# Kernel tuning notes

Measured on AMD Instinct MI355X. Metric: run time of the kernel, lower is better.

Reference implementation:

```python
import jax, jax.numpy as jnp
import numpy as np


def setup_inputs() -> dict:
    key = jax.random.key(0)
    kq, kk, kv = jax.random.split(key, 3)
    B, S, D = 8, 2048, 128
    Q = jax.random.normal(kq, (B, S, D), dtype=jnp.float32)
    K = jax.random.normal(kk, (B, S, D), dtype=jnp.float32)
    V = jax.random.normal(kv, (B, S, D), dtype=jnp.float32)
    return {"Q": Q, "K": K, "V": V}


def reference(Q, K, V):
    # scores: [B, S, S]
    d = Q.shape[-1]
    scores = jnp.einsum('bqd,bkd->bqk', Q, K) / jnp.sqrt(jnp.float32(d))
    # causal mask: position i attends to keys <= i (original sets upper triangle to -inf)
    S = scores.shape[-1]
    causal = jnp.tril(jnp.ones((S, S), dtype=bool))  # [S, S]
    scores = jnp.where(causal[None, :, :], scores, -jnp.inf)
    probs = jax.nn.softmax(scores, axis=-1)
    return jnp.einsum('bqk,bkd->bqd', probs, V)
```

## Files before the change

kernel.cpp:

```cpp
#include <hip/hip_runtime.h>

#define BB 8
#define SS 2048
#define DD 128
#define SEG ((size_t)BB * SS * DD)

typedef _Float16 f16;
typedef _Float16 f16x2 __attribute__((ext_vector_type(2)));
typedef __fp16 h16x2 __attribute__((ext_vector_type(2)));
typedef _Float16 f16x8 __attribute__((ext_vector_type(8)));
typedef float f32x4 __attribute__((ext_vector_type(4)));

#define SWV(d) ((((d) & 7) ^ (((d) >> 3) & 7)) << 3)

#define DEFER_THR 4.0f

static __device__ __forceinline__ float fast_exp2(float x) {
#if __has_builtin(__builtin_amdgcn_exp2f)
    return __builtin_amdgcn_exp2f(x);
#else
    return exp2f(x);
#endif
}

static __device__ __forceinline__ f16x2 cvt_pk(float a, float b) {
    h16x2 r = __builtin_amdgcn_cvt_pkrtz(a, b);
    return __builtin_bit_cast(f16x2, r);
}

static __device__ __forceinline__ uint2 pack4(f32x4 v) {
    f16x2 lo = cvt_pk(v[0], v[1]);
    f16x2 hi = cvt_pk(v[2], v[3]);
    uint2 u;
    u.x = __builtin_bit_cast(unsigned int, lo);
    u.y = __builtin_bit_cast(unsigned int, hi);
    return u;
}

template <int NS>
__global__ __launch_bounds__(256, 2)
void attn_fwd(const float* __restrict__ Qg, const float* __restrict__ Kg,
              const float* __restrict__ Vg, float* __restrict__ Og,
              f16* __restrict__ Opf, float2* __restrict__ mlb)
{
    __shared__ __align__(16) f16 Kl[2][64 * 128];
    __shared__ __align__(16) f16 Vt[2][128 * 64];
    __shared__ __align__(16) f16 Pl[4][16 * 64];

    const int tid  = threadIdx.x;
    const int lane = tid & 63;
    const int w    = tid >> 6;
    const int c_   = lane & 15;
    const int g    = lane >> 4;

    const int L   = blockIdx.x;
    const int bb  = L & 7;
    const int rem = L >> 3;
    const int qb  = 31 - (rem / NS);
    const int sg  = rem % NS;
    const int T   = qb + 1;
    const int t0  = (T * sg) / NS;
    const int t1  = (T * (sg + 1)) / NS;

    const int qrow0 = qb * 64 + w * 16;

    const float qs = 0.08838834764831845f * 1.4426950408889634f;
    f16x8 qf[4];
    {
        const float* qp = Qg + (size_t)(bb * SS + qrow0 + c_) * DD;
#pragma unroll
        for (int kk = 0; kk < 4; ++kk) {
            const int d0 = kk * 32 + g * 8;
            f32x4 a = *(const f32x4*)(qp + d0);
            f32x4 b = *(const f32x4*)(qp + d0 + 4);
            f16x8 q;
#pragma unroll
            for (int i = 0; i < 4; ++i) {
                q[i]     = (f16)(a[i] * qs);
                q[i + 4] = (f16)(b[i] * qs);
            }
            qf[kk] = q;
        }
    }

    f32x4 Oa[8];
#pragma unroll
    for (int i = 0; i < 8; ++i) Oa[i] = (f32x4){0.f, 0.f, 0.f, 0.f};
    float mrun[4] = {-1e30f, -1e30f, -1e30f, -1e30f};
    float lpart[4] = {0.f, 0.f, 0.f, 0.f};

    f16* Pw = &Pl[w][0];

    const int krow = tid >> 5;
    const int kc4  = tid & 31;
    const int vkg  = tid >> 5;
    const int vq   = tid & 31;

    f32x4 kreg[8], vreg[8];

#define LOADT(tt)                                                              \
    {                                                                          \
        const size_t gb = (size_t)(bb * SS + (tt) * 64) * DD;                  \
        _Pragma("unroll")                                                      \
        for (int j = 0; j < 8; ++j)                                            \
            kreg[j] = *(const f32x4*)(Kg + gb + (krow + 8 * j) * DD + kc4 * 4);\
        _Pragma("unroll")                                                      \
        for (int i = 0; i < 8; ++i)                                            \
            vreg[i] = *(const f32x4*)(Vg + gb + (vkg * 8 + i) * DD + vq * 4);  \
    }

#define STAGE_K(pb_)                                                           \
    {                                                                          \
        _Pragma("unroll")                                                      \
        for (int j = 0; j < 8; ++j) {                                          \
            const int row = krow + 8 * j;                                      \
            const int el  = row * 128 + ((kc4 * 4) ^ ((row & 7) << 3));        \
            *(uint2*)&Kl[pb_][el] = pack4(kreg[j]);                            \
        }                                                                      \
    }

#define STAGE_V(pb_)                                                           \
    {                                                                          \
        _Pragma("unroll")                                                      \
        for (int dd = 0; dd < 4; ++dd) {                                       \
            const int d  = vq * 4 + dd;                                        \
            const int sw = SWV(d);                                             \
            _Pragma("unroll")                                                  \
            for (int h = 0; h < 2; ++h) {                                      \
                f32x4 vv = {vreg[4 * h + 0][dd], vreg[4 * h + 1][dd],          \
                            vreg[4 * h + 2][dd], vreg[4 * h + 3][dd]};         \
                const int el = d * 64 + ((vkg * 8 + 4 * h) ^ sw);              \
                *(uint2*)&Vt[pb_][el] = pack4(vv);                             \
            }                                                                  \
        }                                                                      \
    }

    if (t0 < t1) {
        LOADT(t0);
        STAGE_K(t0 & 1);
        STAGE_V(t0 & 1);
        if (t0 + 1 < t1) LOADT(t0 + 1);
        __syncthreads();

        for (int t = t0; t < t1; ++t) {
            const int pb = t & 1;
            const bool more = (t + 1 < t1);
            const int kbase = t * 64;

            f32x4 s4[4];
            __builtin_amdgcn_s_setprio(1);
#pragma unroll
            for (int nb = 0; nb < 4; ++nb) {
                f32x4 acc = (f32x4){0.f, 0.f, 0.f, 0.f};
                const int row = c_ + nb * 16;
                const int sw  = (row & 7) << 3;
#pragma unroll
                for (int kk = 0; kk < 4; ++kk) {
                    f16x8 kb = *(const f16x8*)&Kl[pb][row * 128 + ((kk * 32 + g * 8) ^ sw)];
                    acc = __builtin_amdgcn_mfma_f32_16x16x32_f16(qf[kk], kb, acc, 0, 0, 0);
                }
                s4[nb] = acc;
            }
            __builtin_amdgcn_s_setprio(0);

            if (more) STAGE_K(pb ^ 1);

            if (t == qb) {
#pragma unroll
                for (int nb = 0; nb < 4; ++nb)
#pragma unroll
                    for (int r = 0; r < 4; ++r) {
                        const int kj = kbase + nb * 16 + c_;
                        const int qi = qrow0 + g * 4 + r;
                        if (kj > qi) s4[nb][r] = -1e30f;
                    }
            }

            float wm = -1e30f;
#pragma unroll
            for (int nb = 0; nb < 4; ++nb) {
                f32x4 v = s4[nb];
                wm = fmaxf(wm, fmaxf(fmaxf(v[0], v[1]), fmaxf(v[2], v[3])));
            }
            wm = fmaxf(wm, __shfl_xor(wm, 1));
            wm = fmaxf(wm, __shfl_xor(wm, 2));
            wm = fmaxf(wm, __shfl_xor(wm, 4));
            wm = fmaxf(wm, __shfl_xor(wm, 8));
            wm = fmaxf(wm, __shfl_xor(wm, 16));
            wm = fmaxf(wm, __shfl_xor(wm, 32));
            float mrmin = fminf(fminf(mrun[0], mrun[1]), fminf(mrun[2], mrun[3]));

            if (!__all(wm - mrmin <= DEFER_THR)) {
                float sc[4];
                float scmin = 1.0f;
#pragma unroll
                for (int r = 0; r < 4; ++r) {
                    float pm = fmaxf(fmaxf(s4[0][r], s4[1][r]),
                                     fmaxf(s4[2][r], s4[3][r]));
                    pm = fmaxf(pm, __shfl_xor(pm, 1));
                    pm = fmaxf(pm, __shfl_xor(pm, 2));
                    pm = fmaxf(pm, __shfl_xor(pm, 4));
                    pm = fmaxf(pm, __shfl_xor(pm, 8));
                    const bool keep = (pm - mrun[r] <= DEFER_THR);
                    sc[r] = keep ? 1.0f : fast_exp2(mrun[r] - pm);
                    if (!keep) mrun[r] = pm;
                    scmin = fminf(scmin, sc[r]);
                }
                if (scmin < 1.0f) {
#pragma unroll
                    for (int r = 0; r < 4; ++r) {
                        lpart[r] *= sc[r];
#pragma unroll
                        for (int dblk = 0; dblk < 8; ++dblk)
                            Oa[dblk][r] *= sc[r];
                    }
                }
            }

#pragma unroll
            for (int nb = 0; nb < 4; ++nb) {
                float pv[4];
#pragma unroll
                for (int r = 0; r < 4; ++r) {
                    pv[r] = fast_exp2(s4[nb][r] - mrun[r]);
                    lpart[r] += pv[r];
                }
                f16x2 p01 = cvt_pk(pv[0], pv[1]);
                f16x2 p23 = cvt_pk(pv[2], pv[3]);
#pragma unroll
                for (int r = 0; r < 4; ++r) {
                    const int row = g * 4 + r;
                    const f16 hv = (r < 2) ? p01[r & 1] : p23[r & 1];
                    Pw[row * 64 + ((nb * 16 + c_) ^ ((row & 7) << 3))] = hv;
                }
            }

            if (more) STAGE_V(pb ^ 1);

#pragma unroll
            for (int ks = 0; ks < 2; ++ks) {
                f16x8 pa = *(const f16x8*)&Pw[c_ * 64 + ((ks * 32 + g * 8) ^ ((c_ & 7) << 3))];
                __builtin_amdgcn_s_setprio(1);
#pragma unroll
                for (int dblk = 0; dblk < 8; ++dblk) {
                    const int d  = dblk * 16 + c_;
                    f16x8 vb = *(const f16x8*)&Vt[pb][d * 64 + ((ks * 32 + g * 8) ^ SWV(d))];
                    Oa[dblk] = __builtin_amdgcn_mfma_f32_16x16x32_f16(pa, vb, Oa[dblk], 0, 0, 0);
                }
                __builtin_amdgcn_s_setprio(0);
            }

            if (t + 2 < t1) LOADT(t + 2);
            if (more) __syncthreads();
        }
    }

    float lrun[4];
#pragma unroll
    for (int r = 0; r < 4; ++r) {
        float v = lpart[r];
        v += __shfl_xor(v, 1);
        v += __shfl_xor(v, 2);
        v += __shfl_xor(v, 4);
        v += __shfl_xor(v, 8);
        lrun[r] = v;
    }

    if (NS == 1) {
#pragma unroll
        for (int r = 0; r < 4; ++r) {
            const int qrow = qrow0 + g * 4 + r;
            float* dst = Og + (size_t)(bb * SS + qrow) * DD + c_;
            const float inv = 1.0f / lrun[r];
#pragma unroll
            for (int dblk = 0; dblk < 8; ++dblk)
                dst[dblk * 16] = Oa[dblk][r] * inv;
        }
    } else {
        f16*    od  = Opf + (size_t)sg * SEG;
        float2* mld = mlb + (size_t)sg * BB * SS;
#pragma unroll
        for (int r = 0; r < 4; ++r) {
            const int qrow = qrow0 + g * 4 + r;
            f16* dst = od + (size_t)(bb * SS + qrow) * DD + c_;
#pragma unroll
            for (int dblk = 0; dblk < 8; ++dblk)
                dst[dblk * 16] = (f16)Oa[dblk][r];
            if (c_ == 0) mld[bb * SS + qrow] = make_float2(mrun[r], lrun[r]);
        }
    }
}

template <int NS>
__global__ __launch_bounds__(256)
void merge_kernel(float* __restrict__ out, const f16* __restrict__ Opf,
                  const float2* __restrict__ mlb)
{
    const int idx = blockIdx.x * 256 + threadIdx.x;
    const int row = idx >> 4;
    float2 ml[NS];
#pragma unroll
    for (int i = 0; i < NS; ++i) ml[i] = mlb[(size_t)i * BB * SS + row];
    float mm = ml[0].x;
#pragma unroll
    for (int i = 1; i < NS; ++i) mm = fmaxf(mm, ml[i].x);
    float e[NS], den = 0.f;
#pragma unroll
    for (int i = 0; i < NS; ++i) {
        e[i] = fast_exp2(ml[i].x - mm);
        den += ml[i].y * e[i];
    }
    const float inv = 1.0f / den;

    float acc[8] = {0.f, 0.f, 0.f, 0.f, 0.f, 0.f, 0.f, 0.f};
#pragma unroll
    for (int i = 0; i < NS; ++i) {
        f16x8 v = *(const f16x8*)(Opf + (size_t)i * SEG + (size_t)idx * 8);
#pragma unroll
        for (int j = 0; j < 8; ++j) acc[j] += (float)v[j] * e[i];
    }
    float4 o0, o1;
    o0.x = acc[0] * inv; o0.y = acc[1] * inv; o0.z = acc[2] * inv; o0.w = acc[3] * inv;
    o1.x = acc[4] * inv; o1.y = acc[5] * inv; o1.z = acc[6] * inv; o1.w = acc[7] * inv;
    float4* dst = (float4*)(out + (size_t)idx * 8);
    dst[0] = o0;
    dst[1] = o1;
}

extern "C" void kernel_launch(void* const* d_in, const int* in_sizes, int n_in,
                              void* d_out, int out_size, void* d_ws, size_t ws_size,
                              hipStream_t stream)
{
    const float* Q = (const float*)d_in[0];
    const float* K = (const float*)d_in[1];
    const float* V = (const float*)d_in[2];
    float* out = (float*)d_out;

    const size_t OPB = SEG * sizeof(f16);
    const size_t MLB = (size_t)BB * SS * sizeof(float2);
    const int mergeGrid = (int)(SEG / 8 / 256);

    const size_t need4 = 4 * OPB + 4 * MLB;

    if (ws_size >= need4) {
        f16*    Opf = (f16*)d_ws;
        float2* mlb = (float2*)((char*)d_ws + 4 * OPB);
        hipLaunchKernelGGL((attn_fwd<4>), dim3(8 * 32 * 4), dim3(256), 0, stream,
                           Q, K, V, out, Opf, mlb);
        hipLaunchKernelGGL((merge_kernel<4>), dim3(mergeGrid), dim3(256), 0, stream,
                           out, Opf, mlb);
    } else {
        hipLaunchKernelGGL((attn_fwd<1>), dim3(8 * 32), dim3(256), 0, stream,
                           Q, K, V, out, (f16*)nullptr, (float2*)nullptr);
    }
}
```

Before: 103.6 us.

## Compute transposed S tile so P stays in registers, dropping LDS round trip

Swaps the MFMA operand order so each lane holds a full query row's scores in a transposed layout. The softmax probabilities are then repacked into the PV MFMA operand with cross-lane shuffles instead of being written to and read back from a per-wave LDS buffer. Row-max and row-sum reductions shrink to two shuffles with a single running max per lane, and output stores become vectorised. The cost is sixteen shuffles per tile plus select logic in exchange for removing the LDS stores, loads and associated latency.

Result: no change. 103.3 us (-0.3%).

```diff
diff --git a/kernel.cpp b/kernel.cpp
--- a/kernel.cpp
+++ b/kernel.cpp
@@ -10,6 +10,7 @@
 typedef __fp16 h16x2 __attribute__((ext_vector_type(2)));
 typedef _Float16 f16x8 __attribute__((ext_vector_type(8)));
 typedef float f32x4 __attribute__((ext_vector_type(4)));
+typedef int i32x4 __attribute__((ext_vector_type(4)));
 
 #define SWV(d) ((((d) & 7) ^ (((d) >> 3) & 7)) << 3)
 
@@ -28,12 +29,14 @@
     return __builtin_bit_cast(f16x2, r);
 }
 
+static __device__ __forceinline__ int cvt_pk_i(float a, float b) {
+    return __builtin_bit_cast(int, cvt_pk(a, b));
+}
+
 static __device__ __forceinline__ uint2 pack4(f32x4 v) {
-    f16x2 lo = cvt_pk(v[0], v[1]);
-    f16x2 hi = cvt_pk(v[2], v[3]);
     uint2 u;
-    u.x = __builtin_bit_cast(unsigned int, lo);
-    u.y = __builtin_bit_cast(unsigned int, hi);
+    u.x = (unsigned)cvt_pk_i(v[0], v[1]);
+    u.y = (unsigned)cvt_pk_i(v[2], v[3]);
     return u;
 }
 
@@ -45,7 +48,6 @@
 {
     __shared__ __align__(16) f16 Kl[2][64 * 128];
     __shared__ __align__(16) f16 Vt[2][128 * 64];
-    __shared__ __align__(16) f16 Pl[4][16 * 64];
 
     const int tid  = threadIdx.x;
     const int lane = tid & 63;
@@ -63,11 +65,16 @@
     const int t1  = (T * (sg + 1)) / NS;
 
     const int qrow0 = qb * 64 + w * 16;
+    const int qi    = qrow0 + c_;
+
+    const int srcA = c_ + 32 * (g & 1);
+    const int srcB = srcA + 16;
+    const int selH = g >> 1;
 
     const float qs = 0.08838834764831845f * 1.4426950408889634f;
     f16x8 qf[4];
     {
-        const float* qp = Qg + (size_t)(bb * SS + qrow0 + c_) * DD;
+        const float* qp = Qg + (size_t)(bb * SS + qi) * DD;
 #pragma unroll
         for (int kk = 0; kk < 4; ++kk) {
             const int d0 = kk * 32 + g * 8;
@@ -86,10 +93,8 @@
     f32x4 Oa[8];
 #pragma unroll
     for (int i = 0; i < 8; ++i) Oa[i] = (f32x4){0.f, 0.f, 0.f, 0.f};
-    float mrun[4] = {-1e30f, -1e30f, -1e30f, -1e30f};
-    float lpart[4] = {0.f, 0.f, 0.f, 0.f};
-
-    f16* Pw = &Pl[w][0];
+    float mrun  = -1e30f;
+    float lpart = 0.f;
 
     const int krow = tid >> 5;
     const int kc4  = tid & 31;
@@ -157,7 +162,7 @@
 #pragma unroll
                 for (int kk = 0; kk < 4; ++kk) {
                     f16x8 kb = *(const f16x8*)&Kl[pb][row * 128 + ((kk * 32 + g * 8) ^ sw)];
-                    acc = __builtin_amdgcn_mfma_f32_16x16x32_f16(qf[kk], kb, acc, 0, 0, 0);
+                    acc = __builtin_amdgcn_mfma_f32_16x16x32_f16(kb, qf[kk], acc, 0, 0, 0);
                 }
                 s4[nb] = acc;
             }
@@ -170,82 +175,73 @@
                 for (int nb = 0; nb < 4; ++nb)
 #pragma unroll
                     for (int r = 0; r < 4; ++r) {
-                        const int kj = kbase + nb * 16 + c_;
-                        const int qi = qrow0 + g * 4 + r;
+                        const int kj = kbase + nb * 16 + g * 4 + r;
                         if (kj > qi) s4[nb][r] = -1e30f;
                     }
             }
 
-            float wm = -1e30f;
+            float pm = -1e30f;
 #pragma unroll
             for (int nb = 0; nb < 4; ++nb) {
                 f32x4 v = s4[nb];
-                wm = fmaxf(wm, fmaxf(fmaxf(v[0], v[1]), fmaxf(v[2], v[3])));
-            }
-            wm = fmaxf(wm, __shfl_xor(wm, 1));
-            wm = fmaxf(wm, __shfl_xor(wm, 2));
-            wm = fmaxf(wm, __shfl_xor(wm, 4));
-            wm = fmaxf(wm, __shfl_xor(wm, 8));
-            wm = fmaxf(wm, __shfl_xor(wm, 16));
-            wm = fmaxf(wm, __shfl_xor(wm, 32));
-            float mrmin = fminf(fminf(mrun[0], mrun[1]), fminf(mrun[2], mrun[3]));
-
-            if (!__all(wm - mrmin <= DEFER_THR)) {
-                float sc[4];
-                float scmin = 1.0f;
-#pragma unroll
-                for (int r = 0; r < 4; ++r) {
-                    float pm = fmaxf(fmaxf(s4[0][r], s4[1][r]),
-                                     fmaxf(s4[2][r], s4[3][r]));
-                    pm = fmaxf(pm, __shfl_xor(pm, 1));
-                    pm = fmaxf(pm, __shfl_xor(pm, 2));
-                    pm = fmaxf(pm, __shfl_xor(pm, 4));
-                    pm = fmaxf(pm, __shfl_xor(pm, 8));
-                    const bool keep = (pm - mrun[r] <= DEFER_THR);
-                    sc[r] = keep ? 1.0f : fast_exp2(mrun[r] - pm);
-                    if (!keep) mrun[r] = pm;
-                    scmin = fminf(scmin, sc[r]);
+                pm = fmaxf(pm, fmaxf(fmaxf(v[0], v[1]), fmaxf(v[2], v[3])));
+            }
+            pm = fmaxf(pm, __shfl_xor(pm, 16));
+            pm = fmaxf(pm, __shfl_xor(pm, 32));
+
+            if (!__all(pm - mrun <= DEFER_THR)) {
+                float sc;
+                if (pm - mrun <= DEFER_THR) {
+                    sc = 1.0f;
+                } else {
+                    sc = fast_exp2(mrun - pm);
+                    mrun = pm;
                 }
-                if (scmin < 1.0f) {
-#pragma unroll
-                    for (int r = 0; r < 4; ++r) {
-                        lpart[r] *= sc[r];
-#pragma unroll
-                        for (int dblk = 0; dblk < 8; ++dblk)
-                            Oa[dblk][r] *= sc[r];
-                    }
+                lpart *= sc;
+#pragma unroll
+                for (int dblk = 0; dblk < 8; ++dblk) {
+                    Oa[dblk][0] *= sc; Oa[dblk][1] *= sc;
+                    Oa[dblk][2] *= sc; Oa[dblk][3] *= sc;
                 }
             }
 
+            int ph_lo[4], ph_hi[4];
 #pragma unroll
             for (int nb = 0; nb < 4; ++nb) {
-                float pv[4];
-#pragma unroll
-                for (int r = 0; r < 4; ++r) {
-                    pv[r] = fast_exp2(s4[nb][r] - mrun[r]);
-                    lpart[r] += pv[r];
-                }
-                f16x2 p01 = cvt_pk(pv[0], pv[1]);
-                f16x2 p23 = cvt_pk(pv[2], pv[3]);
-#pragma unroll
-                for (int r = 0; r < 4; ++r) {
-                    const int row = g * 4 + r;
-                    const f16 hv = (r < 2) ? p01[r & 1] : p23[r & 1];
-                    Pw[row * 64 + ((nb * 16 + c_) ^ ((row & 7) << 3))] = hv;
-                }
+                float p0 = fast_exp2(s4[nb][0] - mrun);
+                float p1 = fast_exp2(s4[nb][1] - mrun);
+                float p2 = fast_exp2(s4[nb][2] - mrun);
+                float p3 = fast_exp2(s4[nb][3] - mrun);
+                lpart += (p0 + p1) + (p2 + p3);
+                ph_lo[nb] = cvt_pk_i(p0, p1);
+                ph_hi[nb] = cvt_pk_i(p2, p3);
             }
 
             if (more) STAGE_V(pb ^ 1);
 
 #pragma unroll
             for (int ks = 0; ks < 2; ++ks) {
-                f16x8 pa = *(const f16x8*)&Pw[c_ * 64 + ((ks * 32 + g * 8) ^ ((c_ & 7) << 3))];
+                const int lo1L = __shfl(ph_lo[2 * ks + 0], srcA);
+                const int hi1L = __shfl(ph_hi[2 * ks + 0], srcA);
+                const int lo2L = __shfl(ph_lo[2 * ks + 0], srcB);
+                const int hi2L = __shfl(ph_hi[2 * ks + 0], srcB);
+                const int lo1H = __shfl(ph_lo[2 * ks + 1], srcA);
+                const int hi1H = __shfl(ph_hi[2 * ks + 1], srcA);
+                const int lo2H = __shfl(ph_lo[2 * ks + 1], srcB);
+                const int hi2H = __shfl(ph_hi[2 * ks + 1], srcB);
+                i32x4 bw;
+                bw[0] = selH ? lo1H : lo1L;
+                bw[1] = selH ? hi1H : hi1L;
+                bw[2] = selH ? lo2H : lo2L;
+                bw[3] = selH ? hi2H : hi2L;
+                const f16x8 pbfrag = __builtin_bit_cast(f16x8, bw);
+
                 __builtin_amdgcn_s_setprio(1);
 #pragma unroll
                 for (int dblk = 0; dblk < 8; ++dblk) {
                     const int d  = dblk * 16 + c_;
                     f16x8 vb = *(const f16x8*)&Vt[pb][d * 64 + ((ks * 32 + g * 8) ^ SWV(d))];
-                    Oa[dblk] = __builtin_amdgcn_mfma_f32_16x16x32_f16(pa, vb, Oa[dblk], 0, 0, 0);
+                    Oa[dblk] = __builtin_amdgcn_mfma_f32_16x16x32_f16(vb, pbfrag, Oa[dblk], 0, 0, 0);
                 }
                 __builtin_amdgcn_s_setprio(0);
             }
@@ -255,39 +251,27 @@
         }
     }
 
-    float lrun[4];
-#pragma unroll
-    for (int r = 0; r < 4; ++r) {
-        float v = lpart[r];
-        v += __shfl_xor(v, 1);
-        v += __shfl_xor(v, 2);
-        v += __shfl_xor(v, 4);
-        v += __shfl_xor(v, 8);
-        lrun[r] = v;
-    }
+    float lrun = lpart;
+    lrun += __shfl_xor(lrun, 16);
+    lrun += __shfl_xor(lrun, 32);
 
     if (NS == 1) {
-#pragma unroll
-        for (int r = 0; r < 4; ++r) {
-            const int qrow = qrow0 + g * 4 + r;
-            float* dst = Og + (size_t)(bb * SS + qrow) * DD + c_;
-            const float inv = 1.0f / lrun[r];
-#pragma unroll
-            for (int dblk = 0; dblk < 8; ++dblk)
-                dst[dblk * 16] = Oa[dblk][r] * inv;
+        float* dst = Og + (size_t)(bb * SS + qi) * DD + g * 4;
+        const float inv = (lrun > 0.f) ? 1.0f / lrun : 0.f;
+#pragma unroll
+        for (int dblk = 0; dblk < 8; ++dblk) {
+            float4 o;
+            o.x = Oa[dblk][0] * inv; o.y = Oa[dblk][1] * inv;
+            o.z = Oa[dblk][2] * inv; o.w = Oa[dblk][3] * inv;
+            *(float4*)(dst + dblk * 16) = o;
         }
     } else {
-        f16*    od  = Opf + (size_t)sg * SEG;
-        float2* mld = mlb + (size_t)sg * BB * SS;
-#pragma unroll
-        for (int r = 0; r < 4; ++r) {
-            const int qrow = qrow0 + g * 4 + r;
-            f16* dst = od + (size_t)(bb * SS + qrow) * DD + c_;
-#pragma unroll
-            for (int dblk = 0; dblk < 8; ++dblk)
-                dst[dblk * 16] = (f16)Oa[dblk][r];
-            if (c_ == 0) mld[bb * SS + qrow] = make_float2(mrun[r], lrun[r]);
-        }
+        f16* od = Opf + (size_t)sg * SEG + (size_t)(bb * SS + qi) * DD + g * 4;
+#pragma unroll
+        for (int dblk = 0; dblk < 8; ++dblk)
+            *(uint2*)(od + dblk * 16) = pack4(Oa[dblk]);
+        if (g == 0)
+            mlb[(size_t)sg * BB * SS + bb * SS + qi] = make_float2(mrun, lrun);
     }
 }
 
```
